# Kernel tuning notes

Hardware: AMD Instinct MI355X
Metric: run time of the kernel (lower is better)

## Reference

```python
import jax, jax.numpy as jnp
import numpy as np

DIM = 128
CODEBOOK_SCALE = 16384
N_TOKENS = 16384


def setup_inputs() -> dict:
    key = jax.random.key(0)
    k1, k2 = jax.random.split(key)
    x = jax.random.normal(k1, (N_TOKENS, DIM), dtype=jnp.float32)
    codebook = jax.random.normal(k2, (CODEBOOK_SCALE, DIM), dtype=jnp.float32)
    return {"x": x, "codebook": codebook}


def reference(x, codebook):
    # scores: [N, codebook_scale] = x @ codebook.T
    scores = jnp.einsum("nd,cd->nc", x, codebook)
    indices = jnp.argmax(scores, axis=-1)  # [N] int
    loss = jnp.zeros((), dtype=jnp.float32)  # original returns constant 0.0 loss
    return (indices, loss)
```

## Files before the change

### kernel.cpp

```cpp
#include <hip/hip_runtime.h>
#include <hip/hip_bf16.h>

#define NT 16384
#define ND 128
#define NC 16384
#define NSPLIT 8
#define MARGIN 0.4f

typedef __bf16 bf16x8 __attribute__((ext_vector_type(8)));
typedef unsigned short u16x8 __attribute__((ext_vector_type(8)));
typedef float f32x4 __attribute__((ext_vector_type(4)));

#define MF __builtin_amdgcn_mfma_f32_16x16x32_bf16

static __device__ __forceinline__ unsigned short f2bf(float f) {
    unsigned u = __float_as_uint(f);
    return (unsigned short)((u + 0x7FFFu + ((u >> 16) & 1u)) >> 16);
}
static __device__ __forceinline__ float bf2f(unsigned short u) {
    return __uint_as_float(((unsigned)u) << 16);
}
static __device__ __forceinline__ bf16x8 u2b(u16x8 u) {
    return __builtin_bit_cast(bf16x8, u);
}

__global__ __launch_bounds__(256) void lfq_convert_cb(
    const float4* __restrict__ cb4, unsigned short* __restrict__ cbs)
{
    const unsigned i = blockIdx.x * 256 + threadIdx.x;
    const unsigned c  = i >> 4;
    const unsigned k8 = i & 15u;
    const float4 v0 = cb4[i * 2];
    const float4 v1 = cb4[i * 2 + 1];
    const unsigned split = c >> 11;
    const unsigned cl    = c & 2047u;
    const unsigned pair  = cl >> 5;
    const unsigned sp    = (cl >> 4) & 1u;
    const unsigned n     = cl & 15u;
    const unsigned k     = k8 >> 2;
    const unsigned quad  = k8 & 3u;
    const unsigned idx = split * 262144u + pair * 4096u + sp * 2048u +
                         k * 512u + quad * 128u + n * 8u;
    u16x8 h;
    h[0] = f2bf(v0.x); h[1] = f2bf(v0.y); h[2] = f2bf(v0.z); h[3] = f2bf(v0.w);
    h[4] = f2bf(v1.x); h[5] = f2bf(v1.y); h[6] = f2bf(v1.z); h[7] = f2bf(v1.w);
    *(u16x8*)(cbs + idx) = h;
}

static __device__ __forceinline__ float exact_dot(
    const float4* __restrict__ xr4, const float* __restrict__ cf, int cidx)
{
    const float4* cr = (const float4*)(cf + (size_t)cidx * ND);
    float a0 = 0.f, a1 = 0.f, a2 = 0.f, a3 = 0.f;
#pragma unroll
    for (int i = 0; i < 32; i += 4) {
        float4 x0 = xr4[i+0], x1 = xr4[i+1], x2 = xr4[i+2], x3 = xr4[i+3];
        float4 c0 = cr[i+0],  c1 = cr[i+1],  c2 = cr[i+2],  c3 = cr[i+3];
        a0 += x0.x*c0.x + x0.y*c0.y + x0.z*c0.z + x0.w*c0.w;
        a1 += x1.x*c1.x + x1.y*c1.y + x1.z*c1.z + x1.w*c1.w;
        a2 += x2.x*c2.x + x2.y*c2.y + x2.z*c2.z + x2.w*c2.w;
        a3 += x3.x*c3.x + x3.y*c3.y + x3.z*c3.z + x3.w*c3.w;
    }
    return (a0 + a1) + (a2 + a3);
}

static __device__ __forceinline__ float exact_dot_g(
    const float* __restrict__ xf, const float* __restrict__ cf,
    int token, int cidx)
{
    const float4* xr = (const float4*)(xf + (size_t)token * ND);
    const float4* cr = (const float4*)(cf + (size_t)cidx * ND);
    float a0 = 0.f, a1 = 0.f, a2 = 0.f, a3 = 0.f;
#pragma unroll
    for (int i = 0; i < 32; i += 4) {
        float4 x0 = xr[i+0], x1 = xr[i+1], x2 = xr[i+2], x3 = xr[i+3];
        float4 c0 = cr[i+0], c1 = cr[i+1], c2 = cr[i+2], c3 = cr[i+3];
        a0 += x0.x*c0.x + x0.y*c0.y + x0.z*c0.z + x0.w*c0.w;
        a1 += x1.x*c1.x + x1.y*c1.y + x1.z*c1.z + x1.w*c1.w;
        a2 += x2.x*c2.x + x2.y*c2.y + x2.z*c2.z + x2.w*c2.w;
        a3 += x3.x*c3.x + x3.y*c3.y + x3.z*c3.z + x3.w*c3.w;
    }
    return (a0 + a1) + (a2 + a3);
}

static __device__ __forceinline__ void top2_upd(
    const f32x4& a, float* b1r, float* b2r, unsigned pk)
{
#pragma unroll
    for (int r4 = 0; r4 < 4; ++r4) {
        float p = __uint_as_float((__float_as_uint(a[r4]) & 0xFFFFFF80u) | pk);
        b2r[r4] = __builtin_amdgcn_fmed3f(p, b1r[r4], b2r[r4]);
        b1r[r4] = fmaxf(p, b1r[r4]);
    }
}

__global__ __launch_bounds__(256)
__attribute__((amdgpu_waves_per_eu(2, 2)))
void lfq_stage1(
    const float* __restrict__ xf, const unsigned short* __restrict__ cbs,
    float* __restrict__ sb1, float* __restrict__ sb2,
    int* __restrict__ si1, int* __restrict__ si2)
{
    const int split = blockIdx.x & 7;
    const int tb    = blockIdx.x >> 3;
    const int t0    = tb * 256;
    const int tid   = threadIdx.x;
    const int w     = tid >> 6;
    const int lane  = tid & 63;
    const int n     = lane & 15;
    const int quad  = lane >> 4;

    bf16x8 ah[4][4];
#pragma unroll
    for (int tt = 0; tt < 4; ++tt) {
        const float* xr = xf + (size_t)(t0 + w * 64 + tt * 16 + n) * ND + quad * 8;
#pragma unroll
        for (int kk = 0; kk < 4; ++kk) {
            float4 v0 = *(const float4*)(xr + kk * 32);
            float4 v1 = *(const float4*)(xr + kk * 32 + 4);
            u16x8 hu;
            hu[0] = f2bf(v0.x);
            hu[1] = f2bf(v0.y);
            hu[2] = f2bf(v0.z);
            hu[3] = f2bf(v0.w);
            hu[4] = f2bf(v1.x);
            hu[5] = f2bf(v1.y);
            hu[6] = f2bf(v1.z);
            hu[7] = f2bf(v1.w);
            ah[tt][kk] = u2b(hu);
        }
    }

    float b1[4][4], b2[4][4];
#pragma unroll
    for (int tt = 0; tt < 4; ++tt)
#pragma unroll
        for (int r = 0; r < 4; ++r) { b1[tt][r] = -3.0e38f; b2[tt][r] = -3.0e38f; }

    const unsigned char* gp =
        (const unsigned char*)cbs + (size_t)split * 524288u +
        (unsigned)lane * 16u;

    const f32x4 zq = {0.f, 0.f, 0.f, 0.f};

#define LOADPAIR(Q0,Q1,Q2,Q3,Q4,Q5,Q6,Q7, G)                                   \
    Q0 = *(const bf16x8*)((G));                                                \
    Q1 = *(const bf16x8*)((G) + 1024);                                         \
    Q2 = *(const bf16x8*)((G) + 2048);                                         \
    Q3 = *(const bf16x8*)((G) + 3072);                                         \
    Q4 = *(const bf16x8*)((G) + 4096);                                         \
    Q5 = *(const bf16x8*)((G) + 5120);                                         \
    Q6 = *(const bf16x8*)((G) + 6144);                                         \
    Q7 = *(const bf16x8*)((G) + 7168);

#define COMPUTE(Q0,Q1,Q2,Q3,Q4,Q5,Q6,Q7, P)                                    \
    {                                                                          \
        f32x4 aA0, aA1, aA2, aA3, aB0, aB1, aB2, aB3;                          \
        __builtin_amdgcn_s_setprio(1);                                         \
        aA0 = MF(ah[0][0], Q0, zq,  0,0,0);                                    \
        aA1 = MF(ah[1][0], Q0, zq,  0,0,0);                                    \
        aA2 = MF(ah[2][0], Q0, zq,  0,0,0);                                    \
        aA3 = MF(ah[3][0], Q0, zq,  0,0,0);                                    \
        aB0 = MF(ah[0][0], Q4, zq,  0,0,0);                                    \
        aB1 = MF(ah[1][0], Q4, zq,  0,0,0);                                    \
        aB2 = MF(ah[2][0], Q4, zq,  0,0,0);                                    \
        aB3 = MF(ah[3][0], Q4, zq,  0,0,0);                                    \
        aA0 = MF(ah[0][1], Q1, aA0, 0,0,0);                                    \
        aA1 = MF(ah[1][1], Q1, aA1, 0,0,0);                                    \
        aA2 = MF(ah[2][1], Q1, aA2, 0,0,0);                                    \
        aA3 = MF(ah[3][1], Q1, aA3, 0,0,0);                                    \
        aB0 = MF(ah[0][1], Q5, aB0, 0,0,0);                                    \
        aB1 = MF(ah[1][1], Q5, aB1, 0,0,0);                                    \
        aB2 = MF(ah[2][1], Q5, aB2, 0,0,0);                                    \
        aB3 = MF(ah[3][1], Q5, aB3, 0,0,0);                                    \
        aA0 = MF(ah[0][2], Q2, aA0, 0,0,0);                                    \
        aA1 = MF(ah[1][2], Q2, aA1, 0,0,0);                                    \
        aA2 = MF(ah[2][2], Q2, aA2, 0,0,0);                                    \
        aA3 = MF(ah[3][2], Q2, aA3, 0,0,0);                                    \
        aB0 = MF(ah[0][2], Q6, aB0, 0,0,0);                                    \
        aB1 = MF(ah[1][2], Q6, aB1, 0,0,0);                                    \
        aB2 = MF(ah[2][2], Q6, aB2, 0,0,0);                                    \
        aB3 = MF(ah[3][2], Q6, aB3, 0,0,0);                                    \
        aA0 = MF(ah[0][3], Q3, aA0, 0,0,0);                                    \
        aA1 = MF(ah[1][3], Q3, aA1, 0,0,0);                                    \
        aA2 = MF(ah[2][3], Q3, aA2, 0,0,0);                                    \
        aA3 = MF(ah[3][3], Q3, aA3, 0,0,0);                                    \
        aB0 = MF(ah[0][3], Q7, aB0, 0,0,0);                                    \
        aB1 = MF(ah[1][3], Q7, aB1, 0,0,0);                                    \
        aB2 = MF(ah[2][3], Q7, aB2, 0,0,0);                                    \
        aB3 = MF(ah[3][3], Q7, aB3, 0,0,0);                                    \
        __builtin_amdgcn_s_setprio(0);                                         \
        const unsigned pkA = (unsigned)(127 - (P) * 2);                        \
        const unsigned pkB = (unsigned)(127 - (P) * 2 - 1);                    \
        top2_upd(aA0, b1[0], b2[0], pkA);                                      \
        top2_upd(aA1, b1[1], b2[1], pkA);                                      \
        top2_upd(aA2, b1[2], b2[2], pkA);                                      \
        top2_upd(aA3, b1[3], b2[3], pkA);                                      \
        top2_upd(aB0, b1[0], b2[0], pkB);                                      \
        top2_upd(aB1, b1[1], b2[1], pkB);                                      \
        top2_upd(aB2, b1[2], b2[2], pkB);                                      \
        top2_upd(aB3, b1[3], b2[3], pkB);                                      \
    }

    bf16x8 qa0, qa1, qa2, qa3, qa4, qa5, qa6, qa7;
    bf16x8 qb0, qb1, qb2, qb3, qb4, qb5, qb6, qb7;

    LOADPAIR(qa0,qa1,qa2,qa3,qa4,qa5,qa6,qa7, gp)

    for (int p = 0; p < 62; p += 2) {
        LOADPAIR(qb0,qb1,qb2,qb3,qb4,qb5,qb6,qb7, gp + (p + 1) * 8192)
        COMPUTE (qa0,qa1,qa2,qa3,qa4,qa5,qa6,qa7, p)
        LOADPAIR(qa0,qa1,qa2,qa3,qa4,qa5,qa6,qa7, gp + (p + 2) * 8192)
        COMPUTE (qb0,qb1,qb2,qb3,qb4,qb5,qb6,qb7, p + 1)
    }
    LOADPAIR(qb0,qb1,qb2,qb3,qb4,qb5,qb6,qb7, gp + 63 * 8192)
    COMPUTE (qa0,qa1,qa2,qa3,qa4,qa5,qa6,qa7, 62)
    COMPUTE (qb0,qb1,qb2,qb3,qb4,qb5,qb6,qb7, 63)

#undef LOADPAIR
#undef COMPUTE

    const int cb_base = split * (NC / NSPLIT);
    float v1[4][4], v2[4][4];
    int   c1[4][4], c2[4][4];
#pragma unroll
    for (int tt = 0; tt < 4; ++tt)
#pragma unroll
        for (int r = 0; r < 4; ++r) {
            int j1 = 127 - (int)(__float_as_uint(b1[tt][r]) & 127u);
            int j2 = 127 - (int)(__float_as_uint(b2[tt][r]) & 127u);
            v1[tt][r] = b1[tt][r]; c1[tt][r] = cb_base + j1 * 16 + n;
            v2[tt][r] = b2[tt][r]; c2[tt][r] = cb_base + j2 * 16 + n;
        }

#pragma unroll
    for (int tt = 0; tt < 4; ++tt)
#pragma unroll
        for (int r = 0; r < 4; ++r) {
#pragma unroll
            for (int off = 1; off < 16; off <<= 1) {
                float ob1 = __shfl_xor(v1[tt][r], off, 64);
                int   oi1 = __shfl_xor(c1[tt][r], off, 64);
                float ob2 = __shfl_xor(v2[tt][r], off, 64);
                int   oi2 = __shfl_xor(c2[tt][r], off, 64);
                bool gt = (ob1 > v1[tt][r]) ||
                          (ob1 == v1[tt][r] && oi1 < c1[tt][r]);
                float ls = gt ? v1[tt][r] : ob1;
                int   li = gt ? c1[tt][r] : oi1;
                float ws_ = gt ? ob2 : v2[tt][r];
                int   wi = gt ? oi2 : c2[tt][r];
                bool s2 = (ls > ws_) || (ls == ws_ && li < wi);
                v2[tt][r] = s2 ? ls : ws_;
                c2[tt][r] = s2 ? li : wi;
                v1[tt][r] = gt ? ob1 : v1[tt][r];
                c1[tt][r] = gt ? oi1 : c1[tt][r];
            }
        }

    if (n == 0) {
#pragma unroll
        for (int tt = 0; tt < 4; ++tt)
#pragma unroll
            for (int r = 0; r < 4; ++r) {
                const int token = t0 + w * 64 + tt * 16 + quad * 4 + r;
                const size_t o = (size_t)split * NT + token;
                sb1[o] = v1[tt][r]; si1[o] = c1[tt][r];
                sb2[o] = v2[tt][r]; si2[o] = c2[tt][r];
            }
    }
}

__global__ __launch_bounds__(256) void lfq_combine(
    const float* __restrict__ sb1, const float* __restrict__ sb2,
    const int* __restrict__ si1, const int* __restrict__ si2,
    const float* __restrict__ xf, const float* __restrict__ cf,
    float* __restrict__ out, int out_size)
{
    const int lane = threadIdx.x & 63;
    const int wv   = threadIdx.x >> 6;
    const int g    = lane >> 3;
    const int cl   = lane & 7;
    const int t    = (blockIdx.x * 4 + wv) * 8 + g;

    const size_t o = (size_t)cl * NT + t;
    const float va = sb1[o]; const int ia = si1[o];
    const float vb = sb2[o]; const int ib = si2[o];

    bool lgt = (vb > va) || (vb == va && ib < ia);
    float m  = lgt ? vb : va;
    int   mi = lgt ? ib : ia;
#pragma unroll
    for (int off = 1; off < 8; off <<= 1) {
        float om = __shfl_xor(m, off, 64);
        int   oi = __shfl_xor(mi, off, 64);
        if (om > m || (om == m && oi < mi)) { m = om; mi = oi; }
    }
    const float A1 = m;
    const int   I1 = mi;

    const bool ba = (va >= A1 - MARGIN);
    const bool bb_ = (vb >= A1 - MARGIN);
    int cnt = (ba ? 1 : 0) + (bb_ ? 1 : 0);
#pragma unroll
    for (int off = 1; off < 8; off <<= 1)
        cnt += __shfl_xor(cnt, off, 64);

    int bi = I1;
    if (cnt > 1) {
        float sa = -__builtin_inff(), sb_ = -__builtin_inff();
        if (ba)  sa  = exact_dot_g(xf, cf, t, ia);
        if (bb_) sb_ = exact_dot_g(xf, cf, t, ib);
        bool g2 = (sb_ > sa) || (sb_ == sa && ib < ia);
        float bs = g2 ? sb_ : sa;
        int  bid = g2 ? ib : ia;
#pragma unroll
        for (int off = 1; off < 8; off <<= 1) {
            float os = __shfl_xor(bs, off, 64);
            int   oi = __shfl_xor(bid, off, 64);
            if (os > bs || (os == bs && oi < bid)) { bs = os; bid = oi; }
        }
        bi = bid;
    }
    if (cl == 0) out[t] = (float)bi;
    if (blockIdx.x == 0 && threadIdx.x == 0 && out_size > NT) out[NT] = 0.0f;
}

__global__ __launch_bounds__(512) void lfq_fp32_argmax(
    const float* __restrict__ xf, const float* __restrict__ cf,
    float* __restrict__ out, int out_size)
{
    const int tid = threadIdx.x;
    const int w   = tid >> 6;
    const int tok = tid & 63;
    const int t0  = blockIdx.x * 64;
    __shared__ float s_sc[8][64];
    __shared__ int   s_ix[8][64];

    float4 xr[32];
    const float4* xrow = (const float4*)(xf + (size_t)(t0 + tok) * ND);
#pragma unroll
    for (int i = 0; i < 32; ++i) xr[i] = xrow[i];

    float bs = -__builtin_inff();
    int   bi = 0;
    const int c_begin = w * (NC / 8);
    for (int c = c_begin; c < c_begin + NC / 8; ++c) {
        float s = exact_dot(xr, cf, c);
        if (s > bs) { bs = s; bi = c; }
    }
    s_sc[w][tok] = bs; s_ix[w][tok] = bi;
    __syncthreads();
    if (tid < 64) {
        float bsf = s_sc[0][tid]; int bif = s_ix[0][tid];
#pragma unroll
        for (int ww = 1; ww < 8; ++ww) {
            float s2 = s_sc[ww][tid]; int ii = s_ix[ww][tid];
            if (s2 > bsf || (s2 == bsf && ii < bif)) { bsf = s2; bif = ii; }
        }
        out[t0 + tid] = (float)bif;
    }
    if (blockIdx.x == 0 && tid == 0 && out_size > NT) out[NT] = 0.0f;
}

extern "C" void kernel_launch(void* const* d_in, const int* in_sizes, int n_in,
                              void* d_out, int out_size, void* d_ws, size_t ws_size,
                              hipStream_t stream) {
    const float* x  = (const float*)d_in[0];
    const float* cb = (const float*)d_in[1];
    float* out = (float*)d_out;

    const size_t NCE = (size_t)NC * ND;
    const size_t NEED = NCE * 2 + (size_t)NT * NSPLIT * 4 * 4;
    if (ws_size >= NEED) {
        char* ws = (char*)d_ws;
        unsigned short* cbs = (unsigned short*)ws;
        char* sp = ws + NCE * 2;
        float* sb1 = (float*)sp;
        float* sb2 = (float*)(sp + (size_t)NT * NSPLIT * 4);
        int*   si1 = (int*)  (sp + (size_t)NT * NSPLIT * 8);
        int*   si2 = (int*)  (sp + (size_t)NT * NSPLIT * 12);

        lfq_convert_cb<<<dim3(1024), dim3(256), 0, stream>>>(
            (const float4*)cb, cbs);
        lfq_stage1<<<dim3((NT / 256) * NSPLIT), dim3(256), 0, stream>>>(
            x, cbs, sb1, sb2, si1, si2);
        lfq_combine<<<dim3(NT / 32), dim3(256), 0, stream>>>(
            sb1, sb2, si1, si2, x, cb, out, out_size);
    } else {
        lfq_fp32_argmax<<<dim3(NT / 64), dim3(512), 0, stream>>>(x, cb, out, out_size);
    }
}
```

Measured before the change: 156.8 us.

## Switch stage1 to 32x32x16 bf16 MFMA tiles with matching codebook layout

Replaces the 16x16x32 MFMA tiling with 32x32x16 MFMA instructions, so each wave handles two 32-token row tiles against 32-code column tiles. The codebook conversion kernel is re-laid out to match the new B-operand fragment order, and the top-2 tracking, packed index encoding, cross-lane reduction (now over 32 lanes) and output row mapping are all reworked for the 16-element accumulator. The aim is fewer MFMA issues and less top-2 bookkeeping per score. In exchange the cross-lane reduction grows, accumulator register pressure rises, and the s_setprio hints are dropped.

```diff
diff --git a/kernel.cpp b/kernel.cpp
--- a/kernel.cpp
+++ b/kernel.cpp
@@ -9,16 +9,13 @@
 
 typedef __bf16 bf16x8 __attribute__((ext_vector_type(8)));
 typedef unsigned short u16x8 __attribute__((ext_vector_type(8)));
-typedef float f32x4 __attribute__((ext_vector_type(4)));
-
-#define MF __builtin_amdgcn_mfma_f32_16x16x32_bf16
+typedef float f32x16 __attribute__((ext_vector_type(16)));
+
+#define MF32 __builtin_amdgcn_mfma_f32_32x32x16_bf16
 
 static __device__ __forceinline__ unsigned short f2bf(float f) {
     unsigned u = __float_as_uint(f);
     return (unsigned short)((u + 0x7FFFu + ((u >> 16) & 1u)) >> 16);
-}
-static __device__ __forceinline__ float bf2f(unsigned short u) {
-    return __uint_as_float(((unsigned)u) << 16);
 }
 static __device__ __forceinline__ bf16x8 u2b(u16x8 u) {
     return __builtin_bit_cast(bf16x8, u);
@@ -34,13 +31,12 @@
     const float4 v1 = cb4[i * 2 + 1];
     const unsigned split = c >> 11;
     const unsigned cl    = c & 2047u;
-    const unsigned pair  = cl >> 5;
-    const unsigned sp    = (cl >> 4) & 1u;
-    const unsigned n     = cl & 15u;
-    const unsigned k     = k8 >> 2;
-    const unsigned quad  = k8 & 3u;
-    const unsigned idx = split * 262144u + pair * 4096u + sp * 2048u +
-                         k * 512u + quad * 128u + n * 8u;
+    const unsigned ct    = cl >> 5;
+    const unsigned col   = cl & 31u;
+    const unsigned m     = k8 >> 1;
+    const unsigned half  = k8 & 1u;
+    const unsigned idx = split * 262144u + ct * 4096u + m * 512u +
+                         half * 256u + col * 8u;
     u16x8 h;
     h[0] = f2bf(v0.x); h[1] = f2bf(v0.y); h[2] = f2bf(v0.z); h[3] = f2bf(v0.w);
     h[4] = f2bf(v1.x); h[5] = f2bf(v1.y); h[6] = f2bf(v1.z); h[7] = f2bf(v1.w);
@@ -83,14 +79,14 @@
     return (a0 + a1) + (a2 + a3);
 }
 
-static __device__ __forceinline__ void top2_upd(
-    const f32x4& a, float* b1r, float* b2r, unsigned pk)
-{
-#pragma unroll
-    for (int r4 = 0; r4 < 4; ++r4) {
-        float p = __uint_as_float((__float_as_uint(a[r4]) & 0xFFFFFF80u) | pk);
-        b2r[r4] = __builtin_amdgcn_fmed3f(p, b1r[r4], b2r[r4]);
-        b1r[r4] = fmaxf(p, b1r[r4]);
+static __device__ __forceinline__ void top2_16(
+    const f32x16& a, float* b1r, float* b2r, unsigned pk)
+{
+#pragma unroll
+    for (int r = 0; r < 16; ++r) {
+        float p = __uint_as_float((__float_as_uint(a[r]) & 0xFFFFFF80u) | pk);
+        b2r[r] = __builtin_amdgcn_fmed3f(p, b1r[r], b2r[r]);
+        b1r[r] = fmaxf(p, b1r[r]);
     }
 }
 
@@ -107,17 +103,17 @@
     const int tid   = threadIdx.x;
     const int w     = tid >> 6;
     const int lane  = tid & 63;
-    const int n     = lane & 15;
-    const int quad  = lane >> 4;
-
-    bf16x8 ah[4][4];
-#pragma unroll
-    for (int tt = 0; tt < 4; ++tt) {
-        const float* xr = xf + (size_t)(t0 + w * 64 + tt * 16 + n) * ND + quad * 8;
-#pragma unroll
-        for (int kk = 0; kk < 4; ++kk) {
-            float4 v0 = *(const float4*)(xr + kk * 32);
-            float4 v1 = *(const float4*)(xr + kk * 32 + 4);
+    const int col   = lane & 31;
+    const int half  = lane >> 5;
+
+    bf16x8 ah[2][8];
+#pragma unroll
+    for (int rt = 0; rt < 2; ++rt) {
+        const float* xr = xf + (size_t)(t0 + w * 64 + rt * 32 + col) * ND + half * 8;
+#pragma unroll
+        for (int m = 0; m < 8; ++m) {
+            float4 v0 = *(const float4*)(xr + m * 16);
+            float4 v1 = *(const float4*)(xr + m * 16 + 4);
             u16x8 hu;
             hu[0] = f2bf(v0.x);
             hu[1] = f2bf(v0.y);
@@ -127,145 +123,122 @@
             hu[5] = f2bf(v1.y);
             hu[6] = f2bf(v1.z);
             hu[7] = f2bf(v1.w);
-            ah[tt][kk] = u2b(hu);
-        }
-    }
-
-    float b1[4][4], b2[4][4];
-#pragma unroll
-    for (int tt = 0; tt < 4; ++tt)
-#pragma unroll
-        for (int r = 0; r < 4; ++r) { b1[tt][r] = -3.0e38f; b2[tt][r] = -3.0e38f; }
+            ah[rt][m] = u2b(hu);
+        }
+    }
+
+    float b1[2][16], b2[2][16];
+#pragma unroll
+    for (int rt = 0; rt < 2; ++rt)
+#pragma unroll
+        for (int r = 0; r < 16; ++r) { b1[rt][r] = -3.0e38f; b2[rt][r] = -3.0e38f; }
 
     const unsigned char* gp =
         (const unsigned char*)cbs + (size_t)split * 524288u +
         (unsigned)lane * 16u;
 
-    const f32x4 zq = {0.f, 0.f, 0.f, 0.f};
-
-#define LOADPAIR(Q0,Q1,Q2,Q3,Q4,Q5,Q6,Q7, G)                                   \
-    Q0 = *(const bf16x8*)((G));                                                \
-    Q1 = *(const bf16x8*)((G) + 1024);                                         \
-    Q2 = *(const bf16x8*)((G) + 2048);                                         \
-    Q3 = *(const bf16x8*)((G) + 3072);                                         \
-    Q4 = *(const bf16x8*)((G) + 4096);                                         \
-    Q5 = *(const bf16x8*)((G) + 5120);                                         \
-    Q6 = *(const bf16x8*)((G) + 6144);                                         \
-    Q7 = *(const bf16x8*)((G) + 7168);
-
-#define COMPUTE(Q0,Q1,Q2,Q3,Q4,Q5,Q6,Q7, P)                                    \
+    const f32x16 zq16 = {0.f,0.f,0.f,0.f,0.f,0.f,0.f,0.f,
+                         0.f,0.f,0.f,0.f,0.f,0.f,0.f,0.f};
+
+#define LOADB(Q, G)                                                            \
+    Q##0 = *(const bf16x8*)((G));                                              \
+    Q##1 = *(const bf16x8*)((G) + 1024);                                       \
+    Q##2 = *(const bf16x8*)((G) + 2048);                                       \
+    Q##3 = *(const bf16x8*)((G) + 3072);                                       \
+    Q##4 = *(const bf16x8*)((G) + 4096);                                       \
+    Q##5 = *(const bf16x8*)((G) + 5120);                                       \
+    Q##6 = *(const bf16x8*)((G) + 6144);                                       \
+    Q##7 = *(const bf16x8*)((G) + 7168);
+
+#define CTBODY(Q, CT)                                                          \
     {                                                                          \
-        f32x4 aA0, aA1, aA2, aA3, aB0, aB1, aB2, aB3;                          \
-        __builtin_amdgcn_s_setprio(1);                                         \
-        aA0 = MF(ah[0][0], Q0, zq,  0,0,0);                                    \
-        aA1 = MF(ah[1][0], Q0, zq,  0,0,0);                                    \
-        aA2 = MF(ah[2][0], Q0, zq,  0,0,0);                                    \
-        aA3 = MF(ah[3][0], Q0, zq,  0,0,0);                                    \
-        aB0 = MF(ah[0][0], Q4, zq,  0,0,0);                                    \
-        aB1 = MF(ah[1][0], Q4, zq,  0,0,0);                                    \
-        aB2 = MF(ah[2][0], Q4, zq,  0,0,0);                                    \
-        aB3 = MF(ah[3][0], Q4, zq,  0,0,0);                                    \
-        aA0 = MF(ah[0][1], Q1, aA0, 0,0,0);                                    \
-        aA1 = MF(ah[1][1], Q1, aA1, 0,0,0);                                    \
-        aA2 = MF(ah[2][1], Q1, aA2, 0,0,0);                                    \
-        aA3 = MF(ah[3][1], Q1, aA3, 0,0,0);                                    \
-        aB0 = MF(ah[0][1], Q5, aB0, 0,0,0);                                    \
-        aB1 = MF(ah[1][1], Q5, aB1, 0,0,0);                                    \
-        aB2 = MF(ah[2][1], Q5, aB2, 0,0,0);                                    \
-        aB3 = MF(ah[3][1], Q5, aB3, 0,0,0);                                    \
-        aA0 = MF(ah[0][2], Q2, aA0, 0,0,0);                                    \
-        aA1 = MF(ah[1][2], Q2, aA1, 0,0,0);                                    \
-        aA2 = MF(ah[2][2], Q2, aA2, 0,0,0);                                    \
-        aA3 = MF(ah[3][2], Q2, aA3, 0,0,0);                                    \
-        aB0 = MF(ah[0][2], Q6, aB0, 0,0,0);                                    \
-        aB1 = MF(ah[1][2], Q6, aB1, 0,0,0);                                    \
-        aB2 = MF(ah[2][2], Q6, aB2, 0,0,0);                                    \
-        aB3 = MF(ah[3][2], Q6, aB3, 0,0,0);                                    \
-        aA0 = MF(ah[0][3], Q3, aA0, 0,0,0);                                    \
-        aA1 = MF(ah[1][3], Q3, aA1, 0,0,0);                                    \
-        aA2 = MF(ah[2][3], Q3, aA2, 0,0,0);                                    \
-        aA3 = MF(ah[3][3], Q3, aA3, 0,0,0);                                    \
-        aB0 = MF(ah[0][3], Q7, aB0, 0,0,0);                                    \
-        aB1 = MF(ah[1][3], Q7, aB1, 0,0,0);                                    \
-        aB2 = MF(ah[2][3], Q7, aB2, 0,0,0);                                    \
-        aB3 = MF(ah[3][3], Q7, aB3, 0,0,0);                                    \
-        __builtin_amdgcn_s_setprio(0);                                         \
-        const unsigned pkA = (unsigned)(127 - (P) * 2);                        \
-        const unsigned pkB = (unsigned)(127 - (P) * 2 - 1);                    \
-        top2_upd(aA0, b1[0], b2[0], pkA);                                      \
-        top2_upd(aA1, b1[1], b2[1], pkA);                                      \
-        top2_upd(aA2, b1[2], b2[2], pkA);                                      \
-        top2_upd(aA3, b1[3], b2[3], pkA);                                      \
-        top2_upd(aB0, b1[0], b2[0], pkB);                                      \
-        top2_upd(aB1, b1[1], b2[1], pkB);                                      \
-        top2_upd(aB2, b1[2], b2[2], pkB);                                      \
-        top2_upd(aB3, b1[3], b2[3], pkB);                                      \
+        f32x16 a0, a1;                                                         \
+        a0 = MF32(ah[0][0], Q##0, zq16, 0,0,0);                                \
+        a1 = MF32(ah[1][0], Q##0, zq16, 0,0,0);                                \
+        a0 = MF32(ah[0][1], Q##1, a0,   0,0,0);                                \
+        a1 = MF32(ah[1][1], Q##1, a1,   0,0,0);                                \
+        a0 = MF32(ah[0][2], Q##2, a0,   0,0,0);                                \
+        a1 = MF32(ah[1][2], Q##2, a1,   0,0,0);                                \
+        a0 = MF32(ah[0][3], Q##3, a0,   0,0,0);                                \
+        a1 = MF32(ah[1][3], Q##3, a1,   0,0,0);                                \
+        a0 = MF32(ah[0][4], Q##4, a0,   0,0,0);                                \
+        a1 = MF32(ah[1][4], Q##4, a1,   0,0,0);                                \
+        a0 = MF32(ah[0][5], Q##5, a0,   0,0,0);                                \
+        a1 = MF32(ah[1][5], Q##5, a1,   0,0,0);                                \
+        a0 = MF32(ah[0][6], Q##6, a0,   0,0,0);                                \
+        a1 = MF32(ah[1][6], Q##6, a1,   0,0,0);                                \
+        a0 = MF32(ah[0][7], Q##7, a0,   0,0,0);                                \
+        a1 = MF32(ah[1][7], Q##7, a1,   0,0,0);                                \
+        const unsigned pk = (unsigned)(127 - (CT));                            \
+        top2_16(a0, b1[0], b2[0], pk);                                         \
+        top2_16(a1, b1[1], b2[1], pk);                                         \
     }
 
     bf16x8 qa0, qa1, qa2, qa3, qa4, qa5, qa6, qa7;
     bf16x8 qb0, qb1, qb2, qb3, qb4, qb5, qb6, qb7;
 
-    LOADPAIR(qa0,qa1,qa2,qa3,qa4,qa5,qa6,qa7, gp)
-
-    for (int p = 0; p < 62; p += 2) {
-        LOADPAIR(qb0,qb1,qb2,qb3,qb4,qb5,qb6,qb7, gp + (p + 1) * 8192)
-        COMPUTE (qa0,qa1,qa2,qa3,qa4,qa5,qa6,qa7, p)
-        LOADPAIR(qa0,qa1,qa2,qa3,qa4,qa5,qa6,qa7, gp + (p + 2) * 8192)
-        COMPUTE (qb0,qb1,qb2,qb3,qb4,qb5,qb6,qb7, p + 1)
-    }
-    LOADPAIR(qb0,qb1,qb2,qb3,qb4,qb5,qb6,qb7, gp + 63 * 8192)
-    COMPUTE (qa0,qa1,qa2,qa3,qa4,qa5,qa6,qa7, 62)
-    COMPUTE (qb0,qb1,qb2,qb3,qb4,qb5,qb6,qb7, 63)
-
-#undef LOADPAIR
-#undef COMPUTE
+    LOADB(qa, gp)
+
+    for (int ct = 0; ct < 62; ct += 2) {
+        LOADB(qb, gp + (ct + 1) * 8192)
+        CTBODY(qa, ct)
+        LOADB(qa, gp + (ct + 2) * 8192)
+        CTBODY(qb, ct + 1)
+    }
+    LOADB(qb, gp + 63 * 8192)
+    CTBODY(qa, 62)
+    CTBODY(qb, 63)
+
+#undef LOADB
+#undef CTBODY
 
     const int cb_base = split * (NC / NSPLIT);
-    float v1[4][4], v2[4][4];
-    int   c1[4][4], c2[4][4];
-#pragma unroll
-    for (int tt = 0; tt < 4; ++tt)
-#pragma unroll
-        for (int r = 0; r < 4; ++r) {
-            int j1 = 127 - (int)(__float_as_uint(b1[tt][r]) & 127u);
-            int j2 = 127 - (int)(__float_as_uint(b2[tt][r]) & 127u);
-            v1[tt][r] = b1[tt][r]; c1[tt][r] = cb_base + j1 * 16 + n;
-            v2[tt][r] = b2[tt][r]; c2[tt][r] = cb_base + j2 * 16 + n;
-        }
-
-#pragma unroll
-    for (int tt = 0; tt < 4; ++tt)
-#pragma unroll
-        for (int r = 0; r < 4; ++r) {
-#pragma unroll
-            for (int off = 1; off < 16; off <<= 1) {
-                float ob1 = __shfl_xor(v1[tt][r], off, 64);
-                int   oi1 = __shfl_xor(c1[tt][r], off, 64);
-                float ob2 = __shfl_xor(v2[tt][r], off, 64);
-                int   oi2 = __shfl_xor(c2[tt][r], off, 64);
-                bool gt = (ob1 > v1[tt][r]) ||
-                          (ob1 == v1[tt][r] && oi1 < c1[tt][r]);
-                float ls = gt ? v1[tt][r] : ob1;
-                int   li = gt ? c1[tt][r] : oi1;
-                float ws_ = gt ? ob2 : v2[tt][r];
-                int   wi = gt ? oi2 : c2[tt][r];
+    float v1[2][16], v2[2][16];
+    int   c1[2][16], c2[2][16];
+#pragma unroll
+    for (int rt = 0; rt < 2; ++rt)
+#pragma unroll
+        for (int r = 0; r < 16; ++r) {
+            int j1 = 127 - (int)(__float_as_uint(b1[rt][r]) & 127u);
+            int j2 = 127 - (int)(__float_as_uint(b2[rt][r]) & 127u);
+            v1[rt][r] = b1[rt][r]; c1[rt][r] = cb_base + j1 * 32 + col;
+            v2[rt][r] = b2[rt][r]; c2[rt][r] = cb_base + j2 * 32 + col;
+        }
+
+#pragma unroll
+    for (int rt = 0; rt < 2; ++rt)
+#pragma unroll
+        for (int r = 0; r < 16; ++r) {
+#pragma unroll
+            for (int off = 1; off < 32; off <<= 1) {
+                float ob1 = __shfl_xor(v1[rt][r], off, 64);
+                int   oi1 = __shfl_xor(c1[rt][r], off, 64);
+                float ob2 = __shfl_xor(v2[rt][r], off, 64);
+                int   oi2 = __shfl_xor(c2[rt][r], off, 64);
+                bool gt = (ob1 > v1[rt][r]) ||
+                          (ob1 == v1[rt][r] && oi1 < c1[rt][r]);
+                float ls = gt ? v1[rt][r] : ob1;
+                int   li = gt ? c1[rt][r] : oi1;
+                float ws_ = gt ? ob2 : v2[rt][r];
+                int   wi = gt ? oi2 : c2[rt][r];
                 bool s2 = (ls > ws_) || (ls == ws_ && li < wi);
-                v2[tt][r] = s2 ? ls : ws_;
-                c2[tt][r] = s2 ? li : wi;
-                v1[tt][r] = gt ? ob1 : v1[tt][r];
-                c1[tt][r] = gt ? oi1 : c1[tt][r];
+                v2[rt][r] = s2 ? ls : ws_;
+                c2[rt][r] = s2 ? li : wi;
+                v1[rt][r] = gt ? ob1 : v1[rt][r];
+                c1[rt][r] = gt ? oi1 : c1[rt][r];
             }
         }
 
-    if (n == 0) {
-#pragma unroll
-        for (int tt = 0; tt < 4; ++tt)
-#pragma unroll
-            for (int r = 0; r < 4; ++r) {
-                const int token = t0 + w * 64 + tt * 16 + quad * 4 + r;
-                const size_t o = (size_t)split * NT + token;
-                sb1[o] = v1[tt][r]; si1[o] = c1[tt][r];
-                sb2[o] = v2[tt][r]; si2[o] = c2[tt][r];
+    if (col == 0) {
+#pragma unroll
+        for (int rt = 0; rt < 2; ++rt)
+#pragma unroll
+            for (int r = 0; r < 16; ++r) {
+                const int row   = (r & 3) + 8 * (r >> 2) + 4 * half;
+                const int token = t0 + w * 64 + rt * 32 + row;
+                const size_t o  = (size_t)split * NT + token;
+                sb1[o] = v1[rt][r]; si1[o] = c1[rt][r];
+                sb2[o] = v2[rt][r]; si2[o] = c2[rt][r];
             }
     }
 }
```

Result: slower. 180.7 us (+15.3%).
